# Performance work log

Hardware: AMD Instinct MI355X
Metric: run time of the kernel (lower is better)

Reference implementation:

```python
import jax, jax.numpy as jnp
import numpy as np

N_IN = 100000
N_OUT = 50000
K = 32
E = N_OUT * K
CIN = 16
COUT = 32
KS = 4  # kernel_size per axis


def setup_inputs() -> dict:
    key = jax.random.key(0)
    ks = jax.random.split(key, 8)
    feats = jax.random.normal(ks[0], (N_IN, CIN), jnp.float32)
    inp_points = jax.random.uniform(ks[1], (N_IN, 3), jnp.float32)
    out_points = jax.random.uniform(ks[2], (N_OUT, 3), jnp.float32)
    # voxel size (extent) per output point
    out_extents = 0.1 + 0.1 * jax.random.uniform(ks[3], (N_OUT,), jnp.float32)
    scale_compat = jax.random.uniform(ks[4], (E,), jnp.float32)
    neighbors_index = jax.random.randint(ks[5], (E,), 0, N_IN, jnp.int32)
    # fixed-degree ragged structure: K neighbors per output voxel
    neighbors_row_splits = (jnp.arange(N_OUT + 1) * K).astype(jnp.int32)
    neighbors_distance = jax.random.uniform(ks[6], (E,), jnp.float32)
    kernel = 0.1 * jax.random.normal(ks[7], (KS, KS, KS, CIN, COUT), jnp.float32)
    bias = 0.01 * jax.random.normal(jax.random.fold_in(key, 99), (COUT,), jnp.float32)
    return dict(feats=feats, inp_points=inp_points, out_points=out_points,
                out_extents=out_extents, scale_compat=scale_compat,
                neighbors_index=neighbors_index,
                neighbors_row_splits=neighbors_row_splits,
                neighbors_distance=neighbors_distance, kernel=kernel, bias=bias)


def window_poly6(d):
    # poly6 smoothing window on normalized distance, clamped to [0,1]
    return jnp.clip((1.0 - d * d) ** 3, 0.0, 1.0)


def reference(feats, inp_points, out_points, out_extents, scale_compat,
              neighbors_index, neighbors_row_splits, neighbors_distance,
              kernel, bias):
    E_ = neighbors_index.shape[0]
    n_out = out_points.shape[0]
    cin = feats.shape[1]
    cout = kernel.shape[-1]
    nk = KS * KS * KS  # 64 kernel taps

    # per-edge output id from row_splits
    out_ids = jnp.searchsorted(neighbors_row_splits, jnp.arange(E_), side='right') - 1

    # per-neighbor importance = scale_compat * window_poly6(distance)
    imp = scale_compat * window_poly6(neighbors_distance)

    # relative position normalized to [-1,1] ball (extent is full voxel size)
    rel = (inp_points[neighbors_index] - out_points[out_ids]) / (0.5 * out_extents[out_ids])[:, None]

    # ball_to_cube_radial: radially stretch ball to cube, u = v * ||v||_2 / ||v||_inf
    r = jnp.sqrt(jnp.sum(rel * rel, axis=-1))
    linf = jnp.max(jnp.abs(rel), axis=-1)
    u = rel * (r / jnp.maximum(linf, 1e-12))[:, None]

    # trilinear interpolation coords in kernel grid [0, KS-1]
    t = jnp.clip((u * 0.5 + 0.5) * (KS - 1), 0.0, KS - 1.0)
    t0 = jnp.clip(jnp.floor(t), 0.0, KS - 2.0)
    f = t - t0                      # fractional part, [E,3]
    t0 = t0.astype(jnp.int32)

    # importance-weighted gathered features [E, Cin]
    fe = feats[neighbors_index] * imp[:, None]

    # scatter into per-output per-tap accumulator B [N_out*64, Cin]
    B = jnp.zeros((n_out * nk, cin), feats.dtype)
    for dx in (0, 1):
        wx = f[:, 0] if dx else 1.0 - f[:, 0]
        ix = t0[:, 0] + dx
        for dy in (0, 1):
            wy = f[:, 1] if dy else 1.0 - f[:, 1]
            iy = t0[:, 1] + dy
            for dz in (0, 1):
                wz = f[:, 2] if dz else 1.0 - f[:, 2]
                iz = t0[:, 2] + dz
                w = wx * wy * wz
                kflat = (ix * KS + iy) * KS + iz
                seg = out_ids * nk + kflat
                B = B + jax.ops.segment_sum(fe * w[:, None], seg, num_segments=n_out * nk)

    # contract taps with kernel: [n_out,64,cin] x [64,cin,cout] -> [n_out,cout]
    out = jnp.einsum('nkc,kcd->nd', B.reshape(n_out, nk, cin), kernel.reshape(nk, cin, cout))

    # normalize by summed importance per output point
    den = jax.ops.segment_sum(imp, out_ids, num_segments=n_out)
    out = out / jnp.where(den > 0, den, 1.0)[:, None]

    return jax.nn.relu(out + bias)
```

## Files before the change

kernel.cpp:

```cpp
#include <hip/hip_runtime.h>
#include <hip/hip_fp16.h>

#define NIN 100000
#define NOUT 50000
#define KNB 32
#define CIN 16
#define COUT 32
#define GP 8
#define ROW2B 2064
#define WFOFF 65536

typedef __attribute__((ext_vector_type(8))) _Float16 half8;
typedef __attribute__((ext_vector_type(2))) _Float16 h2v;
typedef __attribute__((ext_vector_type(4))) float f32x4;

__device__ __forceinline__ h2v pmax(h2v a, h2v b) {
  h2v d;
  asm("v_pk_max_f16 %0, %1, %2" : "=v"(d) : "v"(a), "v"(b));
  return d;
}
__device__ __forceinline__ unsigned int pkh(float lo, float hi) {
  union { __half2 h; unsigned int u; } cv;
  cv.h = __floats2half2_rn(lo, hi);
  return cv.u;
}
__device__ __forceinline__ unsigned short f2hbits(float f) {
  union { __half h; unsigned short s; } c; c.h = __float2half_rn(f); return c.s;
}

__global__ void prep_kernel(const float* __restrict__ kern,
                            const float* __restrict__ feats,
                            unsigned short* __restrict__ wf,
                            unsigned short* __restrict__ f16,
                            int do_feats) {
  const int b = blockIdx.x;
  if (b < 128) {
    int idx = b * 256 + threadIdx.x;
    int j = idx & 7;
    int n = (idx >> 3) & 31;
    int g = (idx >> 8) & 3;
    int s = idx >> 10;
    int kc = s * 32 + g * 8 + j;
    wf[idx] = f2hbits(kern[kc * COUT + n]);
  } else if (do_feats) {
    int idx = (b - 128) * 256 + threadIdx.x;
    f16[idx] = f2hbits(feats[idx]);
  }
}

template <int F16F>
__launch_bounds__(256, 8)
__global__ void cconv_kernel(const float* __restrict__ featsf,
                             const unsigned short* __restrict__ feats16,
                             const float* __restrict__ inp_points,
                             const float* __restrict__ out_points,
                             const float* __restrict__ out_extents,
                             const float* __restrict__ scale_compat,
                             const int* __restrict__ nidx,
                             const float* __restrict__ ndist,
                             const unsigned short* __restrict__ wf,
                             const float* __restrict__ bias,
                             float* __restrict__ out) {
  __shared__ __align__(16) char s_bl[GP * ROW2B];
  __shared__ __align__(4) unsigned short s_tx[GP * KNB];
  __shared__ __align__(4) unsigned short s_ty[GP * KNB];
  __shared__ __align__(4) unsigned short s_tz[GP * KNB];
  __shared__ __align__(4) unsigned short s_im[GP * KNB];
  __shared__ float s_cacc[GP][COUT];
  __shared__ float s_den[GP];

  const int tid = threadIdx.x;
  const int wv = tid >> 6;
  const int lane = tid & 63;
  const int c = lane & 15;
  const int g = lane >> 4;

  ((float*)s_cacc)[tid] = 0.0f;

  const int eg0 = blockIdx.x * (GP * KNB) + tid;
  const int my_nb = nidx[eg0];
  const float my_d = ndist[eg0];
  const float my_sc = scale_compat[eg0];
  {
    const int eh = lane >> 1;
    const int hf = lane & 1;
#pragma unroll
    for (int h = 0; h < 2; ++h) {
      const int p = wv * 2 + h;
      const int nb_ = __shfl(my_nb, h * 32 + eh);
      if constexpr (F16F) {
        const uint4 row = *(const uint4*)(feats16 + nb_ * CIN + hf * 8);
        *(uint4*)(s_bl + p * ROW2B + lane * 16) = row;
      } else {
        const float4 r0 = *(const float4*)(featsf + nb_ * CIN + hf * 8);
        const float4 r1 = *(const float4*)(featsf + nb_ * CIN + hf * 8 + 4);
        uint4 rw;
        rw.x = pkh(r0.x, r0.y); rw.y = pkh(r0.z, r0.w);
        rw.z = pkh(r1.x, r1.y); rw.w = pkh(r1.z, r1.w);
        *(uint4*)(s_bl + p * ROW2B + lane * 16) = rw;
      }
    }
  }

  {
    const int h = lane >> 5;
    const int e = lane & 31;
    const int p = wv * 2 + h;
    const int pg = blockIdx.x * GP + p;
    const int nb = my_nb;
    float q = 1.0f - my_d * my_d;
    float w6 = q * q * q;
    w6 = fminf(fmaxf(w6, 0.0f), 1.0f);
    const float imp = my_sc * w6;

    const float inv = 1.0f / (0.5f * out_extents[pg]);
    const float rx = (inp_points[nb * 3 + 0] - out_points[pg * 3 + 0]) * inv;
    const float ry = (inp_points[nb * 3 + 1] - out_points[pg * 3 + 1]) * inv;
    const float rz = (inp_points[nb * 3 + 2] - out_points[pg * 3 + 2]) * inv;
    const float r = sqrtf(rx * rx + ry * ry + rz * rz);
    const float linf = fmaxf(fabsf(rx), fmaxf(fabsf(ry), fabsf(rz)));
    const float sf = r / fmaxf(linf, 1e-12f);
    const float tx = fminf(fmaxf((rx * sf * 0.5f + 0.5f) * 3.0f, 0.0f), 3.0f);
    const float ty = fminf(fmaxf((ry * sf * 0.5f + 0.5f) * 3.0f, 0.0f), 3.0f);
    const float tz = fminf(fmaxf((rz * sf * 0.5f + 0.5f) * 3.0f, 0.0f), 3.0f);

    s_tx[tid] = f2hbits(tx);
    s_ty[tid] = f2hbits(ty);
    s_tz[tid] = f2hbits(tz);
    s_im[tid] = f2hbits(imp);

    float dsum = imp;
#pragma unroll
    for (int m = 1; m < 32; m <<= 1) dsum += __shfl_xor(dsum, m);
    if (e == 0) s_den[p] = dsum;
  }

  {
    const _Float16 kys = (_Float16)(short)(c >> 2);
    const _Float16 kzs = (_Float16)(short)(c & 3);
    const h2v z2 = {(_Float16)0, (_Float16)0};
    const h2v one2 = {(_Float16)1, (_Float16)1};
    const h2v two2 = {(_Float16)2, (_Float16)2};
    const h2v ky2 = {kys, kys};
    const h2v kz2 = {kzs, kzs};
#pragma unroll
    for (int h = 0; h < 2; ++h) {
      const int p = wv * 2 + h;
      union { unsigned int u[4]; h2v h[4]; half8 v; } wfr0, wfr1, wfr2, wfr3, fef;
#pragma unroll
      for (int jp = 0; jp < 4; ++jp) {
        const unsigned a0 = (unsigned)(p * ROW2B + (g * 8 + jp * 2) * 32 + c * 2);
        const unsigned short lo = *(const unsigned short*)(s_bl + a0);
        const unsigned short hi = *(const unsigned short*)(s_bl + a0 + 32);
        fef.u[jp] = (unsigned)lo | ((unsigned)hi << 16);
      }
#pragma unroll
      for (int jp = 0; jp < 4; ++jp) {
        const int eb = p * KNB + g * 8 + jp * 2;
        const h2v tx2 = *(const h2v*)&s_tx[eb];
        const h2v ty2 = *(const h2v*)&s_ty[eb];
        const h2v tz2 = *(const h2v*)&s_tz[eb];
        const h2v im2 = *(const h2v*)&s_im[eb];
        h2v t = ty2 - ky2;
        h2v at = pmax(t, z2 - t);
        const h2v hy = pmax(z2, one2 - at);
        t = tz2 - kz2;
        at = pmax(t, z2 - t);
        const h2v hz = pmax(z2, one2 - at);
        const h2v m2 = hy * hz * im2;
        const h2v w0 = pmax(z2, one2 - tx2) * m2;
        t = tx2 - one2;
        at = pmax(t, z2 - t);
        const h2v w1 = pmax(z2, one2 - at) * m2;
        t = tx2 - two2;
        at = pmax(t, z2 - t);
        const h2v w2 = pmax(z2, one2 - at) * m2;
        const h2v w3 = pmax(z2, t) * m2;
        wfr0.h[jp] = w0;
        wfr1.h[jp] = w1;
        wfr2.h[jp] = w2;
        wfr3.h[jp] = w3;
      }
      const f32x4 z = {0.f, 0.f, 0.f, 0.f};
      f32x4 d0 = __builtin_amdgcn_mfma_f32_16x16x32_f16(fef.v, wfr0.v, z, 0, 0, 0);
      f32x4 d1 = __builtin_amdgcn_mfma_f32_16x16x32_f16(fef.v, wfr1.v, z, 0, 0, 0);
      f32x4 d2 = __builtin_amdgcn_mfma_f32_16x16x32_f16(fef.v, wfr2.v, z, 0, 0, 0);
      f32x4 d3 = __builtin_amdgcn_mfma_f32_16x16x32_f16(fef.v, wfr3.v, z, 0, 0, 0);
      char* bp = s_bl + (unsigned)(p * ROW2B + c * 32 + g * 8);
      *(uint2*)(bp + 0 * 512) = make_uint2(pkh(d0[0], d0[1]), pkh(d0[2], d0[3]));
      *(uint2*)(bp + 1 * 512) = make_uint2(pkh(d1[0], d1[1]), pkh(d1[2], d1[3]));
      *(uint2*)(bp + 2 * 512) = make_uint2(pkh(d2[0], d2[1]), pkh(d2[2], d2[3]));
      *(uint2*)(bp + 3 * 512) = make_uint2(pkh(d3[0], d3[1]), pkh(d3[2], d3[3]));
    }
  }

  __syncthreads();

  f32x4 acc0 = {0.f, 0.f, 0.f, 0.f}, acc1 = {0.f, 0.f, 0.f, 0.f};
  const int pl = lane & 15;
  const int arow = pl & (GP - 1);
  const int g4 = lane >> 4;
#pragma unroll
  for (int ss = 0; ss < 8; ++ss) {
    const int s = wv * 8 + ss;
    const half8 a = *(const half8*)(s_bl + arow * ROW2B + s * 64 + g4 * 16);
    const half8 b0 = *(const half8*)(wf + ((unsigned)((s * 4 + g4) * 32) + pl) * 8);
    const half8 b1 = *(const half8*)(wf + ((unsigned)((s * 4 + g4) * 32) + 16 + pl) * 8);
    acc0 = __builtin_amdgcn_mfma_f32_16x16x32_f16(a, b0, acc0, 0, 0, 0);
    acc1 = __builtin_amdgcn_mfma_f32_16x16x32_f16(a, b1, acc1, 0, 0, 0);
  }
#pragma unroll
  for (int j = 0; j < 4; ++j) {
    const int row = g4 * 4 + j;
    if (row < GP) {
      atomicAdd(&s_cacc[row][pl], acc0[j]);
      atomicAdd(&s_cacc[row][pl + 16], acc1[j]);
    }
  }

  __syncthreads();

  {
    const int p = tid >> 5;
    const int dch = tid & 31;
    const float den = s_den[p];
    float v = ((float*)s_cacc)[tid] / (den > 0.0f ? den : 1.0f) + bias[dch];
    out[blockIdx.x * (GP * COUT) + tid] = fmaxf(v, 0.0f);
  }
}

extern "C" void kernel_launch(void* const* d_in, const int* in_sizes, int n_in,
                              void* d_out, int out_size, void* d_ws, size_t ws_size,
                              hipStream_t stream) {
  const float* feats        = (const float*)d_in[0];
  const float* inp_points   = (const float*)d_in[1];
  const float* out_points   = (const float*)d_in[2];
  const float* out_extents  = (const float*)d_in[3];
  const float* scale_compat = (const float*)d_in[4];
  const int*   nidx         = (const int*)d_in[5];
  const float* ndist        = (const float*)d_in[7];
  const float* kern         = (const float*)d_in[8];
  const float* bias         = (const float*)d_in[9];
  unsigned short* wf  = (unsigned short*)d_ws;
  unsigned short* f16 = (unsigned short*)((char*)d_ws + WFOFF);

  const bool f16ok = ws_size >= (size_t)WFOFF + (size_t)NIN * CIN * 2;
  const int prep_blocks = 128 + (f16ok ? (NIN * CIN) / 256 : 0);
  prep_kernel<<<prep_blocks, 256, 0, stream>>>(kern, feats, wf, f16,
                                               f16ok ? 1 : 0);
  if (f16ok)
    cconv_kernel<1><<<NOUT / GP, 256, 0, stream>>>(feats, f16, inp_points,
        out_points, out_extents, scale_compat, nidx, ndist, wf, bias,
        (float*)d_out);
  else
    cconv_kernel<0><<<NOUT / GP, 256, 0, stream>>>(feats, f16, inp_points,
        out_points, out_extents, scale_compat, nidx, ndist, wf, bias,
        (float*)d_out);
}
```

Baseline: 70.27 us.

## Make conv kernel persistent with register prefetch of next tile's inputs

The kernel now launches a fixed grid of blocks, and each block loops over four output tiles. While the current tile's MFMA work runs, the block issues the next tile's neighbor indices, distances, points and gathered feature values into registers, aiming to hide global gather latency. Feature gathering also changes from a staged LDS row copy to per-lane 16-bit loads packed straight into MFMA operand registers. The trade-off is higher register pressure and smaller, less coalesced gather loads. Out-of-range tiles are clamped to recompute and rewrite the current tile.

```diff
diff --git a/kernel.cpp b/kernel.cpp
--- a/kernel.cpp
+++ b/kernel.cpp
@@ -9,6 +9,9 @@
 #define GP 8
 #define ROW2B 2064
 #define WFOFF 65536
+#define NTILES (NOUT / GP)
+#define PBLK 1563
+#define NITER 4
 
 typedef __attribute__((ext_vector_type(8))) _Float16 half8;
 typedef __attribute__((ext_vector_type(2))) _Float16 h2v;
@@ -47,6 +50,15 @@
     f16[idx] = f2hbits(feats[idx]);
   }
 }
+
+#define GF(dst, nbv, hh, jp)                                                   \
+  { const int n0_ = __shfl(nbv, (hh) * 32 + g * 8 + (jp) * 2);                 \
+    const int n1_ = __shfl(nbv, (hh) * 32 + g * 8 + (jp) * 2 + 1);             \
+    if constexpr (F16F)                                                        \
+      dst = (unsigned)feats16[n0_ * CIN + c]                                   \
+          | ((unsigned)feats16[n1_ * CIN + c] << 16);                          \
+    else                                                                       \
+      dst = pkh(featsf[n0_ * CIN + c], featsf[n1_ * CIN + c]); }
 
 template <int F16F>
 __launch_bounds__(256, 8)
@@ -74,158 +86,186 @@
   const int lane = tid & 63;
   const int c = lane & 15;
   const int g = lane >> 4;
+  const int h1 = lane >> 5;
+  const int e1 = lane & 31;
 
   ((float*)s_cacc)[tid] = 0.0f;
 
-  const int eg0 = blockIdx.x * (GP * KNB) + tid;
-  const int my_nb = nidx[eg0];
-  const float my_d = ndist[eg0];
-  const float my_sc = scale_compat[eg0];
+  int tile = blockIdx.x;
+
+  float dC, scC, pxC, pyC, pzC, oxC, oyC, ozC, invC;
+  unsigned int fC0, fC1, fC2, fC3, fC4, fC5, fC6, fC7;
   {
-    const int eh = lane >> 1;
-    const int hf = lane & 1;
-#pragma unroll
-    for (int h = 0; h < 2; ++h) {
-      const int p = wv * 2 + h;
-      const int nb_ = __shfl(my_nb, h * 32 + eh);
-      if constexpr (F16F) {
-        const uint4 row = *(const uint4*)(feats16 + nb_ * CIN + hf * 8);
-        *(uint4*)(s_bl + p * ROW2B + lane * 16) = row;
-      } else {
-        const float4 r0 = *(const float4*)(featsf + nb_ * CIN + hf * 8);
-        const float4 r1 = *(const float4*)(featsf + nb_ * CIN + hf * 8 + 4);
-        uint4 rw;
-        rw.x = pkh(r0.x, r0.y); rw.y = pkh(r0.z, r0.w);
-        rw.z = pkh(r1.x, r1.y); rw.w = pkh(r1.z, r1.w);
-        *(uint4*)(s_bl + p * ROW2B + lane * 16) = rw;
+    const int e0 = tile * (GP * KNB) + tid;
+    const int nb = nidx[e0];
+    dC = ndist[e0];
+    scC = scale_compat[e0];
+    const int pg = tile * GP + wv * 2 + h1;
+    oxC = out_points[pg * 3 + 0];
+    oyC = out_points[pg * 3 + 1];
+    ozC = out_points[pg * 3 + 2];
+    invC = 1.0f / (0.5f * out_extents[pg]);
+    pxC = inp_points[nb * 3 + 0];
+    pyC = inp_points[nb * 3 + 1];
+    pzC = inp_points[nb * 3 + 2];
+    GF(fC0, nb, 0, 0) GF(fC1, nb, 0, 1) GF(fC2, nb, 0, 2) GF(fC3, nb, 0, 3)
+    GF(fC4, nb, 1, 0) GF(fC5, nb, 1, 1) GF(fC6, nb, 1, 2) GF(fC7, nb, 1, 3)
+  }
+
+#pragma unroll
+  for (int it = 0; it < NITER; ++it) {
+    const int tnraw = tile + PBLK;
+    const int tn = (tnraw < NTILES) ? tnraw : tile;
+
+    int nbN = 0;
+    float dN = 0.f, scN = 0.f, oxN = 0.f, oyN = 0.f, ozN = 0.f, invN = 0.f;
+    if (it + 1 < NITER) {
+      const int e0n = tn * (GP * KNB) + tid;
+      nbN = nidx[e0n];
+      dN = ndist[e0n];
+      scN = scale_compat[e0n];
+      const int pgN = tn * GP + wv * 2 + h1;
+      oxN = out_points[pgN * 3 + 0];
+      oyN = out_points[pgN * 3 + 1];
+      ozN = out_points[pgN * 3 + 2];
+      invN = 1.0f / (0.5f * out_extents[pgN]);
+    }
+
+    {
+      float q = 1.0f - dC * dC;
+      float w6 = q * q * q;
+      w6 = fminf(fmaxf(w6, 0.0f), 1.0f);
+      const float imp = scC * w6;
+      const float rx = (pxC - oxC) * invC;
+      const float ry = (pyC - oyC) * invC;
+      const float rz = (pzC - ozC) * invC;
+      const float r = sqrtf(rx * rx + ry * ry + rz * rz);
+      const float linf = fmaxf(fabsf(rx), fmaxf(fabsf(ry), fabsf(rz)));
+      const float sf = r / fmaxf(linf, 1e-12f);
+      const float tx = fminf(fmaxf((rx * sf * 0.5f + 0.5f) * 3.0f, 0.0f), 3.0f);
+      const float ty = fminf(fmaxf((ry * sf * 0.5f + 0.5f) * 3.0f, 0.0f), 3.0f);
+      const float tz = fminf(fmaxf((rz * sf * 0.5f + 0.5f) * 3.0f, 0.0f), 3.0f);
+
+      s_tx[tid] = f2hbits(tx);
+      s_ty[tid] = f2hbits(ty);
+      s_tz[tid] = f2hbits(tz);
+      s_im[tid] = f2hbits(imp);
+
+      float dsum = imp;
+#pragma unroll
+      for (int m = 1; m < 32; m <<= 1) dsum += __shfl_xor(dsum, m);
+      if (e1 == 0) s_den[wv * 2 + h1] = dsum;
+    }
+
+    {
+      const _Float16 kys = (_Float16)(short)(c >> 2);
+      const _Float16 kzs = (_Float16)(short)(c & 3);
+      const h2v z2 = {(_Float16)0, (_Float16)0};
+      const h2v one2 = {(_Float16)1, (_Float16)1};
+      const h2v two2 = {(_Float16)2, (_Float16)2};
+      const h2v ky2 = {kys, kys};
+      const h2v kz2 = {kzs, kzs};
+#pragma unroll
+      for (int h = 0; h < 2; ++h) {
+        const int p = wv * 2 + h;
+        union { unsigned int u[4]; h2v h[4]; half8 v; } wfr0, wfr1, wfr2, wfr3, fef;
+        if (h == 0) {
+          fef.u[0] = fC0; fef.u[1] = fC1; fef.u[2] = fC2; fef.u[3] = fC3;
+        } else {
+          fef.u[0] = fC4; fef.u[1] = fC5; fef.u[2] = fC6; fef.u[3] = fC7;
+        }
+#pragma unroll
+        for (int jp = 0; jp < 4; ++jp) {
+          const int eb = p * KNB + g * 8 + jp * 2;
+          const h2v tx2 = *(const h2v*)&s_tx[eb];
+          const h2v ty2 = *(const h2v*)&s_ty[eb];
+          const h2v tz2 = *(const h2v*)&s_tz[eb];
+          const h2v im2 = *(const h2v*)&s_im[eb];
+          h2v t = ty2 - ky2;
+          h2v at = pmax(t, z2 - t);
+          const h2v hy = pmax(z2, one2 - at);
+          t = tz2 - kz2;
+          at = pmax(t, z2 - t);
+          const h2v hz = pmax(z2, one2 - at);
+          const h2v m2 = hy * hz * im2;
+          const h2v w0 = pmax(z2, one2 - tx2) * m2;
+          t = tx2 - one2;
+          at = pmax(t, z2 - t);
+          const h2v w1 = pmax(z2, one2 - at) * m2;
+          t = tx2 - two2;
+          at = pmax(t, z2 - t);
+          const h2v w2 = pmax(z2, one2 - at) * m2;
+          const h2v w3 = pmax(z2, t) * m2;
+          wfr0.h[jp] = w0;
+          wfr1.h[jp] = w1;
+          wfr2.h[jp] = w2;
+          wfr3.h[jp] = w3;
+        }
+        const f32x4 z = {0.f, 0.f, 0.f, 0.f};
+        f32x4 d0 = __builtin_amdgcn_mfma_f32_16x16x32_f16(fef.v, wfr0.v, z, 0, 0, 0);
+        f32x4 d1 = __builtin_amdgcn_mfma_f32_16x16x32_f16(fef.v, wfr1.v, z, 0, 0, 0);
+        f32x4 d2 = __builtin_amdgcn_mfma_f32_16x16x32_f16(fef.v, wfr2.v, z, 0, 0, 0);
+        f32x4 d3 = __builtin_amdgcn_mfma_f32_16x16x32_f16(fef.v, wfr3.v, z, 0, 0, 0);
+        char* bp = s_bl + (unsigned)(p * ROW2B + c * 32 + g * 8);
+        *(uint2*)(bp + 0 * 512) = make_uint2(pkh(d0[0], d0[1]), pkh(d0[2], d0[3]));
+        *(uint2*)(bp + 1 * 512) = make_uint2(pkh(d1[0], d1[1]), pkh(d1[2], d1[3]));
+        *(uint2*)(bp + 2 * 512) = make_uint2(pkh(d2[0], d2[1]), pkh(d2[2], d2[3]));
+        *(uint2*)(bp + 3 * 512) = make_uint2(pkh(d3[0], d3[1]), pkh(d3[2], d3[3]));
       }
     }
-  }
-
-  {
-    const int h = lane >> 5;
-    const int e = lane & 31;
-    const int p = wv * 2 + h;
-    const int pg = blockIdx.x * GP + p;
-    const int nb = my_nb;
-    float q = 1.0f - my_d * my_d;
-    float w6 = q * q * q;
-    w6 = fminf(fmaxf(w6, 0.0f), 1.0f);
-    const float imp = my_sc * w6;
-
-    const float inv = 1.0f / (0.5f * out_extents[pg]);
-    const float rx = (inp_points[nb * 3 + 0] - out_points[pg * 3 + 0]) * inv;
-    const float ry = (inp_points[nb * 3 + 1] - out_points[pg * 3 + 1]) * inv;
-    const float rz = (inp_points[nb * 3 + 2] - out_points[pg * 3 + 2]) * inv;
-    const float r = sqrtf(rx * rx + ry * ry + rz * rz);
-    const float linf = fmaxf(fabsf(rx), fmaxf(fabsf(ry), fabsf(rz)));
-    const float sf = r / fmaxf(linf, 1e-12f);
-    const float tx = fminf(fmaxf((rx * sf * 0.5f + 0.5f) * 3.0f, 0.0f), 3.0f);
-    const float ty = fminf(fmaxf((ry * sf * 0.5f + 0.5f) * 3.0f, 0.0f), 3.0f);
-    const float tz = fminf(fmaxf((rz * sf * 0.5f + 0.5f) * 3.0f, 0.0f), 3.0f);
-
-    s_tx[tid] = f2hbits(tx);
-    s_ty[tid] = f2hbits(ty);
-    s_tz[tid] = f2hbits(tz);
-    s_im[tid] = f2hbits(imp);
-
-    float dsum = imp;
-#pragma unroll
-    for (int m = 1; m < 32; m <<= 1) dsum += __shfl_xor(dsum, m);
-    if (e == 0) s_den[p] = dsum;
-  }
-
-  {
-    const _Float16 kys = (_Float16)(short)(c >> 2);
-    const _Float16 kzs = (_Float16)(short)(c & 3);
-    const h2v z2 = {(_Float16)0, (_Float16)0};
-    const h2v one2 = {(_Float16)1, (_Float16)1};
-    const h2v two2 = {(_Float16)2, (_Float16)2};
-    const h2v ky2 = {kys, kys};
-    const h2v kz2 = {kzs, kzs};
-#pragma unroll
-    for (int h = 0; h < 2; ++h) {
-      const int p = wv * 2 + h;
-      union { unsigned int u[4]; h2v h[4]; half8 v; } wfr0, wfr1, wfr2, wfr3, fef;
-#pragma unroll
-      for (int jp = 0; jp < 4; ++jp) {
-        const unsigned a0 = (unsigned)(p * ROW2B + (g * 8 + jp * 2) * 32 + c * 2);
-        const unsigned short lo = *(const unsigned short*)(s_bl + a0);
-        const unsigned short hi = *(const unsigned short*)(s_bl + a0 + 32);
-        fef.u[jp] = (unsigned)lo | ((unsigned)hi << 16);
+
+    __syncthreads();
+
+    float pxN = 0.f, pyN = 0.f, pzN = 0.f;
+    unsigned int fN0 = 0, fN1 = 0, fN2 = 0, fN3 = 0,
+                 fN4 = 0, fN5 = 0, fN6 = 0, fN7 = 0;
+    if (it + 1 < NITER) {
+      pxN = inp_points[nbN * 3 + 0];
+      pyN = inp_points[nbN * 3 + 1];
+      pzN = inp_points[nbN * 3 + 2];
+      GF(fN0, nbN, 0, 0) GF(fN1, nbN, 0, 1) GF(fN2, nbN, 0, 2) GF(fN3, nbN, 0, 3)
+      GF(fN4, nbN, 1, 0) GF(fN5, nbN, 1, 1) GF(fN6, nbN, 1, 2) GF(fN7, nbN, 1, 3)
+    }
+
+    f32x4 acc0 = {0.f, 0.f, 0.f, 0.f}, acc1 = {0.f, 0.f, 0.f, 0.f};
+    const int pl = lane & 15;
+    const int arow = pl & (GP - 1);
+    const int g4 = lane >> 4;
+#pragma unroll
+    for (int ss = 0; ss < 8; ++ss) {
+      const int s = wv * 8 + ss;
+      const half8 a = *(const half8*)(s_bl + arow * ROW2B + s * 64 + g4 * 16);
+      const half8 b0 = *(const half8*)(wf + ((unsigned)((s * 4 + g4) * 32) + pl) * 8);
+      const half8 b1 = *(const half8*)(wf + ((unsigned)((s * 4 + g4) * 32) + 16 + pl) * 8);
+      acc0 = __builtin_amdgcn_mfma_f32_16x16x32_f16(a, b0, acc0, 0, 0, 0);
+      acc1 = __builtin_amdgcn_mfma_f32_16x16x32_f16(a, b1, acc1, 0, 0, 0);
+    }
+#pragma unroll
+    for (int j = 0; j < 4; ++j) {
+      const int row = g4 * 4 + j;
+      if (row < GP) {
+        atomicAdd(&s_cacc[row][pl], acc0[j]);
+        atomicAdd(&s_cacc[row][pl + 16], acc1[j]);
       }
-#pragma unroll
-      for (int jp = 0; jp < 4; ++jp) {
-        const int eb = p * KNB + g * 8 + jp * 2;
-        const h2v tx2 = *(const h2v*)&s_tx[eb];
-        const h2v ty2 = *(const h2v*)&s_ty[eb];
-        const h2v tz2 = *(const h2v*)&s_tz[eb];
-        const h2v im2 = *(const h2v*)&s_im[eb];
-        h2v t = ty2 - ky2;
-        h2v at = pmax(t, z2 - t);
-        const h2v hy = pmax(z2, one2 - at);
-        t = tz2 - kz2;
-        at = pmax(t, z2 - t);
-        const h2v hz = pmax(z2, one2 - at);
-        const h2v m2 = hy * hz * im2;
-        const h2v w0 = pmax(z2, one2 - tx2) * m2;
-        t = tx2 - one2;
-        at = pmax(t, z2 - t);
-        const h2v w1 = pmax(z2, one2 - at) * m2;
-        t = tx2 - two2;
-        at = pmax(t, z2 - t);
-        const h2v w2 = pmax(z2, one2 - at) * m2;
-        const h2v w3 = pmax(z2, t) * m2;
-        wfr0.h[jp] = w0;
-        wfr1.h[jp] = w1;
-        wfr2.h[jp] = w2;
-        wfr3.h[jp] = w3;
-      }
-      const f32x4 z = {0.f, 0.f, 0.f, 0.f};
-      f32x4 d0 = __builtin_amdgcn_mfma_f32_16x16x32_f16(fef.v, wfr0.v, z, 0, 0, 0);
-      f32x4 d1 = __builtin_amdgcn_mfma_f32_16x16x32_f16(fef.v, wfr1.v, z, 0, 0, 0);
-      f32x4 d2 = __builtin_amdgcn_mfma_f32_16x16x32_f16(fef.v, wfr2.v, z, 0, 0, 0);
-      f32x4 d3 = __builtin_amdgcn_mfma_f32_16x16x32_f16(fef.v, wfr3.v, z, 0, 0, 0);
-      char* bp = s_bl + (unsigned)(p * ROW2B + c * 32 + g * 8);
-      *(uint2*)(bp + 0 * 512) = make_uint2(pkh(d0[0], d0[1]), pkh(d0[2], d0[3]));
-      *(uint2*)(bp + 1 * 512) = make_uint2(pkh(d1[0], d1[1]), pkh(d1[2], d1[3]));
-      *(uint2*)(bp + 2 * 512) = make_uint2(pkh(d2[0], d2[1]), pkh(d2[2], d2[3]));
-      *(uint2*)(bp + 3 * 512) = make_uint2(pkh(d3[0], d3[1]), pkh(d3[2], d3[3]));
-    }
-  }
-
-  __syncthreads();
-
-  f32x4 acc0 = {0.f, 0.f, 0.f, 0.f}, acc1 = {0.f, 0.f, 0.f, 0.f};
-  const int pl = lane & 15;
-  const int arow = pl & (GP - 1);
-  const int g4 = lane >> 4;
-#pragma unroll
-  for (int ss = 0; ss < 8; ++ss) {
-    const int s = wv * 8 + ss;
-    const half8 a = *(const half8*)(s_bl + arow * ROW2B + s * 64 + g4 * 16);
-    const half8 b0 = *(const half8*)(wf + ((unsigned)((s * 4 + g4) * 32) + pl) * 8);
-    const half8 b1 = *(const half8*)(wf + ((unsigned)((s * 4 + g4) * 32) + 16 + pl) * 8);
-    acc0 = __builtin_amdgcn_mfma_f32_16x16x32_f16(a, b0, acc0, 0, 0, 0);
-    acc1 = __builtin_amdgcn_mfma_f32_16x16x32_f16(a, b1, acc1, 0, 0, 0);
-  }
-#pragma unroll
-  for (int j = 0; j < 4; ++j) {
-    const int row = g4 * 4 + j;
-    if (row < GP) {
-      atomicAdd(&s_cacc[row][pl], acc0[j]);
-      atomicAdd(&s_cacc[row][pl + 16], acc1[j]);
-    }
-  }
-
-  __syncthreads();
-
-  {
-    const int p = tid >> 5;
-    const int dch = tid & 31;
-    const float den = s_den[p];
-    float v = ((float*)s_cacc)[tid] / (den > 0.0f ? den : 1.0f) + bias[dch];
-    out[blockIdx.x * (GP * COUT) + tid] = fmaxf(v, 0.0f);
+    }
+
+    __syncthreads();
+
+    {
+      const int p = tid >> 5;
+      const int dch = tid & 31;
+      const float den = s_den[p];
+      float v = ((float*)s_cacc)[tid] / (den > 0.0f ? den : 1.0f) + bias[dch];
+      out[tile * (GP * COUT) + tid] = fmaxf(v, 0.0f);
+      ((float*)s_cacc)[tid] = 0.0f;
+    }
+
+    tile = tn;
+    dC = dN; scC = scN;
+    pxC = pxN; pyC = pyN; pzC = pzN;
+    oxC = oxN; oyC = oyN; ozC = ozN; invC = invN;
+    fC0 = fN0; fC1 = fN1; fC2 = fN2; fC3 = fN3;
+    fC4 = fN4; fC5 = fN5; fC6 = fN6; fC7 = fN7;
   }
 }
 
@@ -249,11 +289,11 @@
   prep_kernel<<<prep_blocks, 256, 0, stream>>>(kern, feats, wf, f16,
                                                f16ok ? 1 : 0);
   if (f16ok)
-    cconv_kernel<1><<<NOUT / GP, 256, 0, stream>>>(feats, f16, inp_points,
+    cconv_kernel<1><<<PBLK, 256, 0, stream>>>(feats, f16, inp_points,
         out_points, out_extents, scale_compat, nidx, ndist, wf, bias,
         (float*)d_out);
   else
-    cconv_kernel<0><<<NOUT / GP, 256, 0, stream>>>(feats, f16, inp_points,
+    cconv_kernel<0><<<PBLK, 256, 0, stream>>>(feats, f16, inp_points,
         out_points, out_extents, scale_compat, nidx, ndist, wf, bias,
         (float*)d_out);
 }
```

After: 117.5 us. 67.2% more time.

## Split geometry and feature gather into separate pass before tile MFMA kernel

Applied to the files above, without the earlier changes.

Adds a geom_kernel that computes per-edge tap coordinates and importance, packs them as fp16, and writes the gathered fp16 neighbor features contiguously to workspace. A new tile_kernel then reads these in a streaming, coalesced way instead of doing random gathers. The fallback cconv_kernel is also changed to gather features directly into registers instead of staging them in LDS. The split path costs an extra launch and roughly 60 MB of additional global writes and reads, and it only runs if the workspace is large enough.

```diff
diff --git a/kernel.cpp b/kernel.cpp
--- a/kernel.cpp
+++ b/kernel.cpp
@@ -8,7 +8,12 @@
 #define COUT 32
 #define GP 8
 #define ROW2B 2064
-#define WFOFF 65536
+#define EDG (NOUT * KNB)
+#define WFOFF 0
+#define F16OFF 65536
+#define GMOFF (F16OFF + NIN * CIN * 2)
+#define FEOFF (GMOFF + EDG * 8)
+#define WSNEED ((size_t)FEOFF + (size_t)EDG * CIN * 2)
 
 typedef __attribute__((ext_vector_type(8))) _Float16 half8;
 typedef __attribute__((ext_vector_type(2))) _Float16 h2v;
@@ -26,6 +31,9 @@
 }
 __device__ __forceinline__ unsigned short f2hbits(float f) {
   union { __half h; unsigned short s; } c; c.h = __float2half_rn(f); return c.s;
+}
+__device__ __forceinline__ float hbits2f(unsigned short s) {
+  union { __half h; unsigned short s; } c; c.s = s; return __half2float(c.h);
 }
 
 __global__ void prep_kernel(const float* __restrict__ kern,
@@ -47,6 +55,192 @@
     f16[idx] = f2hbits(feats[idx]);
   }
 }
+
+__launch_bounds__(256)
+__global__ void geom_kernel(const unsigned short* __restrict__ feats16,
+                            const float* __restrict__ inp_points,
+                            const float* __restrict__ out_points,
+                            const float* __restrict__ out_extents,
+                            const float* __restrict__ scale_compat,
+                            const int* __restrict__ nidx,
+                            const float* __restrict__ ndist,
+                            uint2* __restrict__ geom,
+                            unsigned short* __restrict__ fe16) {
+  const int e = blockIdx.x * 256 + threadIdx.x;
+  const int p = e >> 5;
+  const int nb = nidx[e];
+
+  const uint4 r0 = *(const uint4*)(feats16 + nb * CIN);
+  const uint4 r1 = *(const uint4*)(feats16 + nb * CIN + 8);
+
+  const float d = ndist[e];
+  float q = 1.0f - d * d;
+  float w6 = q * q * q;
+  w6 = fminf(fmaxf(w6, 0.0f), 1.0f);
+  const float imp = scale_compat[e] * w6;
+
+  const float inv = 1.0f / (0.5f * out_extents[p]);
+  const float rx = (inp_points[nb * 3 + 0] - out_points[p * 3 + 0]) * inv;
+  const float ry = (inp_points[nb * 3 + 1] - out_points[p * 3 + 1]) * inv;
+  const float rz = (inp_points[nb * 3 + 2] - out_points[p * 3 + 2]) * inv;
+  const float r = sqrtf(rx * rx + ry * ry + rz * rz);
+  const float linf = fmaxf(fabsf(rx), fmaxf(fabsf(ry), fabsf(rz)));
+  const float sf = r / fmaxf(linf, 1e-12f);
+  const float tx = fminf(fmaxf((rx * sf * 0.5f + 0.5f) * 3.0f, 0.0f), 3.0f);
+  const float ty = fminf(fmaxf((ry * sf * 0.5f + 0.5f) * 3.0f, 0.0f), 3.0f);
+  const float tz = fminf(fmaxf((rz * sf * 0.5f + 0.5f) * 3.0f, 0.0f), 3.0f);
+
+  geom[e] = make_uint2(pkh(tx, ty), pkh(tz, imp));
+  *(uint4*)(fe16 + e * CIN) = r0;
+  *(uint4*)(fe16 + e * CIN + 8) = r1;
+}
+
+__launch_bounds__(256, 8)
+__global__ void tile_kernel(const uint2* __restrict__ geom,
+                            const unsigned short* __restrict__ fe16,
+                            const unsigned short* __restrict__ wf,
+                            const float* __restrict__ bias,
+                            float* __restrict__ out) {
+  __shared__ __align__(16) char s_bl[GP * ROW2B];
+  __shared__ __align__(4) unsigned short s_tx[GP * KNB];
+  __shared__ __align__(4) unsigned short s_ty[GP * KNB];
+  __shared__ __align__(4) unsigned short s_tz[GP * KNB];
+  __shared__ __align__(4) unsigned short s_im[GP * KNB];
+  __shared__ float s_cacc[GP][COUT];
+  __shared__ float s_den[GP];
+
+  const int tid = threadIdx.x;
+  const int wv = tid >> 6;
+  const int lane = tid & 63;
+  const int c = lane & 15;
+  const int g = lane >> 4;
+
+  ((float*)s_cacc)[tid] = 0.0f;
+
+  {
+    const int e0 = blockIdx.x * (GP * KNB) + tid;
+    const uint2 gm = geom[e0];
+    const uint4 q0 = *(const uint4*)(fe16 + e0 * CIN);
+    const uint4 q1 = *(const uint4*)(fe16 + e0 * CIN + 8);
+
+    s_tx[tid] = (unsigned short)(gm.x & 0xffffu);
+    s_ty[tid] = (unsigned short)(gm.x >> 16);
+    s_tz[tid] = (unsigned short)(gm.y & 0xffffu);
+    s_im[tid] = (unsigned short)(gm.y >> 16);
+
+    const int p = tid >> 5;
+    const int e2 = tid & 31;
+    *(uint4*)(s_bl + p * ROW2B + e2 * 32) = q0;
+    *(uint4*)(s_bl + p * ROW2B + e2 * 32 + 16) = q1;
+
+    float dsum = hbits2f((unsigned short)(gm.y >> 16));
+#pragma unroll
+    for (int m = 1; m < 32; m <<= 1) dsum += __shfl_xor(dsum, m);
+    if (e2 == 0) s_den[p] = dsum;
+  }
+
+  {
+    const _Float16 kys = (_Float16)(short)(c >> 2);
+    const _Float16 kzs = (_Float16)(short)(c & 3);
+    const h2v z2 = {(_Float16)0, (_Float16)0};
+    const h2v one2 = {(_Float16)1, (_Float16)1};
+    const h2v two2 = {(_Float16)2, (_Float16)2};
+    const h2v ky2 = {kys, kys};
+    const h2v kz2 = {kzs, kzs};
+#pragma unroll
+    for (int h = 0; h < 2; ++h) {
+      const int p = wv * 2 + h;
+      union { unsigned int u[4]; h2v h[4]; half8 v; } wfr0, wfr1, wfr2, wfr3, fef;
+#pragma unroll
+      for (int jp = 0; jp < 4; ++jp) {
+        const unsigned a0 = (unsigned)(p * ROW2B + (g * 8 + jp * 2) * 32 + c * 2);
+        const unsigned short lo = *(const unsigned short*)(s_bl + a0);
+        const unsigned short hi = *(const unsigned short*)(s_bl + a0 + 32);
+        fef.u[jp] = (unsigned)lo | ((unsigned)hi << 16);
+      }
+#pragma unroll
+      for (int jp = 0; jp < 4; ++jp) {
+        const int eb = p * KNB + g * 8 + jp * 2;
+        const h2v tx2 = *(const h2v*)&s_tx[eb];
+        const h2v ty2 = *(const h2v*)&s_ty[eb];
+        const h2v tz2 = *(const h2v*)&s_tz[eb];
+        const h2v im2 = *(const h2v*)&s_im[eb];
+        h2v t = ty2 - ky2;
+        h2v at = pmax(t, z2 - t);
+        const h2v hy = pmax(z2, one2 - at);
+        t = tz2 - kz2;
+        at = pmax(t, z2 - t);
+        const h2v hz = pmax(z2, one2 - at);
+        const h2v m2 = hy * hz * im2;
+        const h2v w0 = pmax(z2, one2 - tx2) * m2;
+        t = tx2 - one2;
+        at = pmax(t, z2 - t);
+        const h2v w1 = pmax(z2, one2 - at) * m2;
+        t = tx2 - two2;
+        at = pmax(t, z2 - t);
+        const h2v w2 = pmax(z2, one2 - at) * m2;
+        const h2v w3 = pmax(z2, t) * m2;
+        wfr0.h[jp] = w0;
+        wfr1.h[jp] = w1;
+        wfr2.h[jp] = w2;
+        wfr3.h[jp] = w3;
+      }
+      const f32x4 z = {0.f, 0.f, 0.f, 0.f};
+      f32x4 d0 = __builtin_amdgcn_mfma_f32_16x16x32_f16(fef.v, wfr0.v, z, 0, 0, 0);
+      f32x4 d1 = __builtin_amdgcn_mfma_f32_16x16x32_f16(fef.v, wfr1.v, z, 0, 0, 0);
+      f32x4 d2 = __builtin_amdgcn_mfma_f32_16x16x32_f16(fef.v, wfr2.v, z, 0, 0, 0);
+      f32x4 d3 = __builtin_amdgcn_mfma_f32_16x16x32_f16(fef.v, wfr3.v, z, 0, 0, 0);
+      char* bp = s_bl + (unsigned)(p * ROW2B + c * 32 + g * 8);
+      *(uint2*)(bp + 0 * 512) = make_uint2(pkh(d0[0], d0[1]), pkh(d0[2], d0[3]));
+      *(uint2*)(bp + 1 * 512) = make_uint2(pkh(d1[0], d1[1]), pkh(d1[2], d1[3]));
+      *(uint2*)(bp + 2 * 512) = make_uint2(pkh(d2[0], d2[1]), pkh(d2[2], d2[3]));
+      *(uint2*)(bp + 3 * 512) = make_uint2(pkh(d3[0], d3[1]), pkh(d3[2], d3[3]));
+    }
+  }
+
+  __syncthreads();
+
+  f32x4 acc0 = {0.f, 0.f, 0.f, 0.f}, acc1 = {0.f, 0.f, 0.f, 0.f};
+  const int pl = lane & 15;
+  const int arow = pl & (GP - 1);
+  const int g4 = lane >> 4;
+#pragma unroll
+  for (int ss = 0; ss < 8; ++ss) {
+    const int s = wv * 8 + ss;
+    const half8 a = *(const half8*)(s_bl + arow * ROW2B + s * 64 + g4 * 16);
+    const half8 b0 = *(const half8*)(wf + ((unsigned)((s * 4 + g4) * 32) + pl) * 8);
+    const half8 b1 = *(const half8*)(wf + ((unsigned)((s * 4 + g4) * 32) + 16 + pl) * 8);
+    acc0 = __builtin_amdgcn_mfma_f32_16x16x32_f16(a, b0, acc0, 0, 0, 0);
+    acc1 = __builtin_amdgcn_mfma_f32_16x16x32_f16(a, b1, acc1, 0, 0, 0);
+  }
+#pragma unroll
+  for (int j = 0; j < 4; ++j) {
+    const int row = g4 * 4 + j;
+    if (row < GP) {
+      atomicAdd(&s_cacc[row][pl], acc0[j]);
+      atomicAdd(&s_cacc[row][pl + 16], acc1[j]);
+    }
+  }
+
+  __syncthreads();
+
+  {
+    const int p = tid >> 5;
+    const int dch = tid & 31;
+    const float den = s_den[p];
+    float v = ((float*)s_cacc)[tid] / (den > 0.0f ? den : 1.0f) + bias[dch];
+    out[blockIdx.x * (GP * COUT) + tid] = fmaxf(v, 0.0f);
+  }
+}
+
+#define GF(dst, nbv, hh, jp)                                                   \
+  { const int n0_ = __shfl(nbv, (hh) * 32 + g * 8 + (jp) * 2);                 \
+    const int n1_ = __shfl(nbv, (hh) * 32 + g * 8 + (jp) * 2 + 1);             \
+    if constexpr (F16F)                                                        \
+      dst = (unsigned)feats16[n0_ * CIN + c]                                   \
+          | ((unsigned)feats16[n1_ * CIN + c] << 16);                          \
+    else                                                                       \
+      dst = pkh(featsf[n0_ * CIN + c], featsf[n1_ * CIN + c]); }
 
 template <int F16F>
 __launch_bounds__(256, 8)
@@ -81,60 +275,40 @@
   const int my_nb = nidx[eg0];
   const float my_d = ndist[eg0];
   const float my_sc = scale_compat[eg0];
-  {
-    const int eh = lane >> 1;
-    const int hf = lane & 1;
-#pragma unroll
-    for (int h = 0; h < 2; ++h) {
-      const int p = wv * 2 + h;
-      const int nb_ = __shfl(my_nb, h * 32 + eh);
-      if constexpr (F16F) {
-        const uint4 row = *(const uint4*)(feats16 + nb_ * CIN + hf * 8);
-        *(uint4*)(s_bl + p * ROW2B + lane * 16) = row;
-      } else {
-        const float4 r0 = *(const float4*)(featsf + nb_ * CIN + hf * 8);
-        const float4 r1 = *(const float4*)(featsf + nb_ * CIN + hf * 8 + 4);
-        uint4 rw;
-        rw.x = pkh(r0.x, r0.y); rw.y = pkh(r0.z, r0.w);
-        rw.z = pkh(r1.x, r1.y); rw.w = pkh(r1.z, r1.w);
-        *(uint4*)(s_bl + p * ROW2B + lane * 16) = rw;
-      }
-    }
-  }
-
+  unsigned int fp[8];
+#pragma unroll
+  for (int h = 0; h < 2; ++h) {
+    GF(fp[h * 4 + 0], my_nb, h, 0) GF(fp[h * 4 + 1], my_nb, h, 1)
+    GF(fp[h * 4 + 2], my_nb, h, 2) GF(fp[h * 4 + 3], my_nb, h, 3)
+  }
   {
     const int h = lane >> 5;
     const int e = lane & 31;
     const int p = wv * 2 + h;
     const int pg = blockIdx.x * GP + p;
-    const int nb = my_nb;
     float q = 1.0f - my_d * my_d;
     float w6 = q * q * q;
     w6 = fminf(fmaxf(w6, 0.0f), 1.0f);
     const float imp = my_sc * w6;
-
     const float inv = 1.0f / (0.5f * out_extents[pg]);
-    const float rx = (inp_points[nb * 3 + 0] - out_points[pg * 3 + 0]) * inv;
-    const float ry = (inp_points[nb * 3 + 1] - out_points[pg * 3 + 1]) * inv;
-    const float rz = (inp_points[nb * 3 + 2] - out_points[pg * 3 + 2]) * inv;
+    const float rx = (inp_points[my_nb * 3 + 0] - out_points[pg * 3 + 0]) * inv;
+    const float ry = (inp_points[my_nb * 3 + 1] - out_points[pg * 3 + 1]) * inv;
+    const float rz = (inp_points[my_nb * 3 + 2] - out_points[pg * 3 + 2]) * inv;
     const float r = sqrtf(rx * rx + ry * ry + rz * rz);
     const float linf = fmaxf(fabsf(rx), fmaxf(fabsf(ry), fabsf(rz)));
     const float sf = r / fmaxf(linf, 1e-12f);
     const float tx = fminf(fmaxf((rx * sf * 0.5f + 0.5f) * 3.0f, 0.0f), 3.0f);
     const float ty = fminf(fmaxf((ry * sf * 0.5f + 0.5f) * 3.0f, 0.0f), 3.0f);
     const float tz = fminf(fmaxf((rz * sf * 0.5f + 0.5f) * 3.0f, 0.0f), 3.0f);
-
     s_tx[tid] = f2hbits(tx);
     s_ty[tid] = f2hbits(ty);
     s_tz[tid] = f2hbits(tz);
     s_im[tid] = f2hbits(imp);
-
     float dsum = imp;
 #pragma unroll
     for (int m = 1; m < 32; m <<= 1) dsum += __shfl_xor(dsum, m);
     if (e == 0) s_den[p] = dsum;
   }
-
   {
     const _Float16 kys = (_Float16)(short)(c >> 2);
     const _Float16 kzs = (_Float16)(short)(c & 3);
@@ -147,13 +321,8 @@
     for (int h = 0; h < 2; ++h) {
       const int p = wv * 2 + h;
       union { unsigned int u[4]; h2v h[4]; half8 v; } wfr0, wfr1, wfr2, wfr3, fef;
-#pragma unroll
-      for (int jp = 0; jp < 4; ++jp) {
-        const unsigned a0 = (unsigned)(p * ROW2B + (g * 8 + jp * 2) * 32 + c * 2);
-        const unsigned short lo = *(const unsigned short*)(s_bl + a0);
-        const unsigned short hi = *(const unsigned short*)(s_bl + a0 + 32);
-        fef.u[jp] = (unsigned)lo | ((unsigned)hi << 16);
-      }
+      fef.u[0] = fp[h * 4 + 0]; fef.u[1] = fp[h * 4 + 1];
+      fef.u[2] = fp[h * 4 + 2]; fef.u[3] = fp[h * 4 + 3];
 #pragma unroll
       for (int jp = 0; jp < 4; ++jp) {
         const int eb = p * KNB + g * 8 + jp * 2;
@@ -176,10 +345,7 @@
         at = pmax(t, z2 - t);
         const h2v w2 = pmax(z2, one2 - at) * m2;
         const h2v w3 = pmax(z2, t) * m2;
-        wfr0.h[jp] = w0;
-        wfr1.h[jp] = w1;
-        wfr2.h[jp] = w2;
-        wfr3.h[jp] = w3;
+        wfr0.h[jp] = w0; wfr1.h[jp] = w1; wfr2.h[jp] = w2; wfr3.h[jp] = w3;
       }
       const f32x4 z = {0.f, 0.f, 0.f, 0.f};
       f32x4 d0 = __builtin_amdgcn_mfma_f32_16x16x32_f16(fef.v, wfr0.v, z, 0, 0, 0);
@@ -193,9 +359,7 @@
       *(uint2*)(bp + 3 * 512) = make_uint2(pkh(d3[0], d3[1]), pkh(d3[2], d3[3]));
     }
   }
-
   __syncthreads();
-
   f32x4 acc0 = {0.f, 0.f, 0.f, 0.f}, acc1 = {0.f, 0.f, 0.f, 0.f};
   const int pl = lane & 15;
   const int arow = pl & (GP - 1);
@@ -217,9 +381,7 @@
       atomicAdd(&s_cacc[row][pl + 16], acc1[j]);
     }
   }
-
   __syncthreads();
-
   {
     const int p = tid >> 5;
     const int dch = tid & 31;
@@ -242,18 +404,27 @@
   const float* kern         = (const float*)d_in[8];
   const float* bias         = (const float*)d_in[9];
   unsigned short* wf  = (unsigned short*)d_ws;
-  unsigned short* f16 = (unsigned short*)((char*)d_ws + WFOFF);
-
-  const bool f16ok = ws_size >= (size_t)WFOFF + (size_t)NIN * CIN * 2;
+  unsigned short* f16 = (unsigned short*)((char*)d_ws + F16OFF);
+  uint2*          gm  = (uint2*)((char*)d_ws + GMOFF);
+  unsigned short* fe  = (unsigned short*)((char*)d_ws + FEOFF);
+
+  const bool f16ok = ws_size >= (size_t)F16OFF + (size_t)NIN * CIN * 2;
+  const bool split = ws_size >= WSNEED;
   const int prep_blocks = 128 + (f16ok ? (NIN * CIN) / 256 : 0);
   prep_kernel<<<prep_blocks, 256, 0, stream>>>(kern, feats, wf, f16,
                                                f16ok ? 1 : 0);
-  if (f16ok)
+  if (split) {
+    geom_kernel<<<EDG / 256, 256, 0, stream>>>(f16, inp_points, out_points,
+                                               out_extents, scale_compat,
+                                               nidx, ndist, gm, fe);
+    tile_kernel<<<NOUT / GP, 256, 0, stream>>>(gm, fe, wf, bias, (float*)d_out);
+  } else if (f16ok) {
     cconv_kernel<1><<<NOUT / GP, 256, 0, stream>>>(feats, f16, inp_points,
         out_points, out_extents, scale_compat, nidx, ndist, wf, bias,
         (float*)d_out);
-  else
+  } else {
     cconv_kernel<0><<<NOUT / GP, 256, 0, stream>>>(feats, f16, inp_points,
         out_points, out_extents, scale_compat, nidx, ndist, wf, bias,
         (float*)d_out);
-}
+  }
+}
```

Result: slower. 97.29 us (+38.5%).

## Process 16 output points per 512-thread block with channel-major LDS feature layout

Applied to the files above, without the earlier changes.

Doubles the output points per block from 8 to 16 and the block size to 512 threads. The second-stage MFMA can then use all 16 A-rows instead of duplicating 8, which halves the per-block tap-contraction work relative to points processed. Gathered neighbor features are now written to LDS channel-major by each edge thread. That lets the first-stage MFMA load its operand as one 16-byte vector read instead of eight scalar 16-bit reads. In exchange, LDS use per block doubles and the global gather becomes per-thread row loads with scattered 2-byte LDS stores.

```diff
diff --git a/kernel.cpp b/kernel.cpp
--- a/kernel.cpp
+++ b/kernel.cpp
@@ -6,7 +6,7 @@
 #define KNB 32
 #define CIN 16
 #define COUT 32
-#define GP 8
+#define GP 16
 #define ROW2B 2064
 #define WFOFF 65536
 
@@ -49,7 +49,7 @@
 }
 
 template <int F16F>
-__launch_bounds__(256, 8)
+__launch_bounds__(512, 8)
 __global__ void cconv_kernel(const float* __restrict__ featsf,
                              const unsigned short* __restrict__ feats16,
                              const float* __restrict__ inp_points,
@@ -74,6 +74,8 @@
   const int lane = tid & 63;
   const int c = lane & 15;
   const int g = lane >> 4;
+  const int p0 = tid >> 5;
+  const int e2 = tid & 31;
 
   ((float*)s_cacc)[tid] = 0.0f;
 
@@ -82,41 +84,34 @@
   const float my_d = ndist[eg0];
   const float my_sc = scale_compat[eg0];
   {
-    const int eh = lane >> 1;
-    const int hf = lane & 1;
-#pragma unroll
-    for (int h = 0; h < 2; ++h) {
-      const int p = wv * 2 + h;
-      const int nb_ = __shfl(my_nb, h * 32 + eh);
-      if constexpr (F16F) {
-        const uint4 row = *(const uint4*)(feats16 + nb_ * CIN + hf * 8);
-        *(uint4*)(s_bl + p * ROW2B + lane * 16) = row;
-      } else {
-        const float4 r0 = *(const float4*)(featsf + nb_ * CIN + hf * 8);
-        const float4 r1 = *(const float4*)(featsf + nb_ * CIN + hf * 8 + 4);
-        uint4 rw;
-        rw.x = pkh(r0.x, r0.y); rw.y = pkh(r0.z, r0.w);
-        rw.z = pkh(r1.x, r1.y); rw.w = pkh(r1.z, r1.w);
-        *(uint4*)(s_bl + p * ROW2B + lane * 16) = rw;
+    char* fetp = s_bl + p0 * ROW2B + e2 * 2;
+    if constexpr (F16F) {
+      union { uint4 q; unsigned short s[8]; } r0, r1;
+      r0.q = *(const uint4*)(feats16 + my_nb * CIN);
+      r1.q = *(const uint4*)(feats16 + my_nb * CIN + 8);
+#pragma unroll
+      for (int cc = 0; cc < 8; ++cc) {
+        *(unsigned short*)(fetp + cc * 64) = r0.s[cc];
+        *(unsigned short*)(fetp + (cc + 8) * 64) = r1.s[cc];
       }
+    } else {
+#pragma unroll
+      for (int cc = 0; cc < 16; ++cc)
+        *(unsigned short*)(fetp + cc * 64) = f2hbits(featsf[my_nb * CIN + cc]);
     }
   }
 
   {
-    const int h = lane >> 5;
-    const int e = lane & 31;
-    const int p = wv * 2 + h;
-    const int pg = blockIdx.x * GP + p;
-    const int nb = my_nb;
+    const int pg = blockIdx.x * GP + p0;
     float q = 1.0f - my_d * my_d;
     float w6 = q * q * q;
     w6 = fminf(fmaxf(w6, 0.0f), 1.0f);
     const float imp = my_sc * w6;
 
     const float inv = 1.0f / (0.5f * out_extents[pg]);
-    const float rx = (inp_points[nb * 3 + 0] - out_points[pg * 3 + 0]) * inv;
-    const float ry = (inp_points[nb * 3 + 1] - out_points[pg * 3 + 1]) * inv;
-    const float rz = (inp_points[nb * 3 + 2] - out_points[pg * 3 + 2]) * inv;
+    const float rx = (inp_points[my_nb * 3 + 0] - out_points[pg * 3 + 0]) * inv;
+    const float ry = (inp_points[my_nb * 3 + 1] - out_points[pg * 3 + 1]) * inv;
+    const float rz = (inp_points[my_nb * 3 + 2] - out_points[pg * 3 + 2]) * inv;
     const float r = sqrtf(rx * rx + ry * ry + rz * rz);
     const float linf = fmaxf(fabsf(rx), fmaxf(fabsf(ry), fabsf(rz)));
     const float sf = r / fmaxf(linf, 1e-12f);
@@ -132,7 +127,7 @@
     float dsum = imp;
 #pragma unroll
     for (int m = 1; m < 32; m <<= 1) dsum += __shfl_xor(dsum, m);
-    if (e == 0) s_den[p] = dsum;
+    if (e2 == 0) s_den[p0] = dsum;
   }
 
   {
@@ -146,14 +141,8 @@
 #pragma unroll
     for (int h = 0; h < 2; ++h) {
       const int p = wv * 2 + h;
-      union { unsigned int u[4]; h2v h[4]; half8 v; } wfr0, wfr1, wfr2, wfr3, fef;
-#pragma unroll
-      for (int jp = 0; jp < 4; ++jp) {
-        const unsigned a0 = (unsigned)(p * ROW2B + (g * 8 + jp * 2) * 32 + c * 2);
-        const unsigned short lo = *(const unsigned short*)(s_bl + a0);
-        const unsigned short hi = *(const unsigned short*)(s_bl + a0 + 32);
-        fef.u[jp] = (unsigned)lo | ((unsigned)hi << 16);
-      }
+      const half8 fefv = *(const half8*)(s_bl + p * ROW2B + c * 64 + g * 16);
+      union { unsigned int u[4]; h2v h[4]; half8 v; } wfr0, wfr1, wfr2, wfr3;
 #pragma unroll
       for (int jp = 0; jp < 4; ++jp) {
         const int eb = p * KNB + g * 8 + jp * 2;
@@ -182,10 +171,10 @@
         wfr3.h[jp] = w3;
       }
       const f32x4 z = {0.f, 0.f, 0.f, 0.f};
-      f32x4 d0 = __builtin_amdgcn_mfma_f32_16x16x32_f16(fef.v, wfr0.v, z, 0, 0, 0);
-      f32x4 d1 = __builtin_amdgcn_mfma_f32_16x16x32_f16(fef.v, wfr1.v, z, 0, 0, 0);
-      f32x4 d2 = __builtin_amdgcn_mfma_f32_16x16x32_f16(fef.v, wfr2.v, z, 0, 0, 0);
-      f32x4 d3 = __builtin_amdgcn_mfma_f32_16x16x32_f16(fef.v, wfr3.v, z, 0, 0, 0);
+      f32x4 d0 = __builtin_amdgcn_mfma_f32_16x16x32_f16(fefv, wfr0.v, z, 0, 0, 0);
+      f32x4 d1 = __builtin_amdgcn_mfma_f32_16x16x32_f16(fefv, wfr1.v, z, 0, 0, 0);
+      f32x4 d2 = __builtin_amdgcn_mfma_f32_16x16x32_f16(fefv, wfr2.v, z, 0, 0, 0);
+      f32x4 d3 = __builtin_amdgcn_mfma_f32_16x16x32_f16(fefv, wfr3.v, z, 0, 0, 0);
       char* bp = s_bl + (unsigned)(p * ROW2B + c * 32 + g * 8);
       *(uint2*)(bp + 0 * 512) = make_uint2(pkh(d0[0], d0[1]), pkh(d0[2], d0[3]));
       *(uint2*)(bp + 1 * 512) = make_uint2(pkh(d1[0], d1[1]), pkh(d1[2], d1[3]));
@@ -198,12 +187,11 @@
 
   f32x4 acc0 = {0.f, 0.f, 0.f, 0.f}, acc1 = {0.f, 0.f, 0.f, 0.f};
   const int pl = lane & 15;
-  const int arow = pl & (GP - 1);
   const int g4 = lane >> 4;
 #pragma unroll
-  for (int ss = 0; ss < 8; ++ss) {
-    const int s = wv * 8 + ss;
-    const half8 a = *(const half8*)(s_bl + arow * ROW2B + s * 64 + g4 * 16);
+  for (int ss = 0; ss < 4; ++ss) {
+    const int s = wv * 4 + ss;
+    const half8 a = *(const half8*)(s_bl + pl * ROW2B + s * 64 + g4 * 16);
     const half8 b0 = *(const half8*)(wf + ((unsigned)((s * 4 + g4) * 32) + pl) * 8);
     const half8 b1 = *(const half8*)(wf + ((unsigned)((s * 4 + g4) * 32) + 16 + pl) * 8);
     acc0 = __builtin_amdgcn_mfma_f32_16x16x32_f16(a, b0, acc0, 0, 0, 0);
@@ -212,10 +200,8 @@
 #pragma unroll
   for (int j = 0; j < 4; ++j) {
     const int row = g4 * 4 + j;
-    if (row < GP) {
-      atomicAdd(&s_cacc[row][pl], acc0[j]);
-      atomicAdd(&s_cacc[row][pl + 16], acc1[j]);
-    }
+    atomicAdd(&s_cacc[row][pl], acc0[j]);
+    atomicAdd(&s_cacc[row][pl + 16], acc1[j]);
   }
 
   __syncthreads();
@@ -249,11 +235,11 @@
   prep_kernel<<<prep_blocks, 256, 0, stream>>>(kern, feats, wf, f16,
                                                f16ok ? 1 : 0);
   if (f16ok)
-    cconv_kernel<1><<<NOUT / GP, 256, 0, stream>>>(feats, f16, inp_points,
+    cconv_kernel<1><<<NOUT / GP, 512, 0, stream>>>(feats, f16, inp_points,
         out_points, out_extents, scale_compat, nidx, ndist, wf, bias,
         (float*)d_out);
   else
-    cconv_kernel<0><<<NOUT / GP, 256, 0, stream>>>(feats, f16, inp_points,
+    cconv_kernel<0><<<NOUT / GP, 512, 0, stream>>>(feats, f16, inp_points,
         out_points, out_extents, scale_compat, nidx, ndist, wf, bias,
         (float*)d_out);
 }
```

Result: slower. 104.8 us (+49.1%).
